# Kernel optimization log

Measured on AMD Instinct MI355X. Metric: run time of the kernel, lower is better.

Reference implementation:

```python
import jax, jax.numpy as jnp
import numpy as np

# geomloss SamplesLoss(loss='sinkhorn') defaults: p=2, blur=0.05, scaling=0.5, debias=True
BLUR = 0.05
P = 2
SCALING = 0.5
EPS_TGT = BLUR ** P            # target temperature = blur^p = 0.0025
EPS_START = 4.0                # ~ diameter^p / p for N(0,1) 3D clouds
N_FINAL = 5                    # extra iterations at target epsilon


def _eps_schedule():
    # static epsilon-annealing schedule (scaling=0.5 => eps *= 0.25 per step for p=2)
    eps, lst = EPS_START, []
    while eps > EPS_TGT:
        lst.append(eps)
        eps *= SCALING ** P
    lst += [EPS_TGT] * N_FINAL
    return jnp.asarray(lst, dtype=jnp.float32)


def _sqcost(x, y):
    # C_ij = ||x_i - y_j||^2 / 2   (geomloss p=2 cost)
    x2 = jnp.sum(x * x, axis=-1)
    y2 = jnp.sum(y * y, axis=-1)
    return 0.5 * (x2[:, None] + y2[None, :] - 2.0 * (x @ y.T))


def _ot_eps(C):
    # log-domain Sinkhorn with epsilon annealing; uniform weights
    N, M = C.shape
    la = -jnp.log(jnp.float32(N))   # log alpha_i
    lb = -jnp.log(jnp.float32(M))   # log beta_j
    f0 = jnp.zeros((N,), dtype=C.dtype)
    g0 = jnp.zeros((M,), dtype=C.dtype)

    def step(carry, eps):
        f, g = carry
        f = -eps * jax.scipy.special.logsumexp(lb + (g[None, :] - C) / eps, axis=1)
        g = -eps * jax.scipy.special.logsumexp(la + (f[:, None] - C) / eps, axis=0)
        return (f, g), None

    (f, g), _ = jax.lax.scan(jax.checkpoint(step), (f0, g0), _eps_schedule())
    # OT_eps(alpha, beta) = <alpha, f> + <beta, g> with uniform weights
    return jnp.mean(f) + jnp.mean(g)


def setup_inputs() -> dict:
    key = jax.random.key(0)
    kx, ky = jax.random.split(key)
    x = jax.random.normal(kx, (4096, 3), dtype=jnp.float32)
    y = jax.random.normal(ky, (4096, 3), dtype=jnp.float32)
    return {"x": x, "y": y}


def reference(x, y):
    # debiased Sinkhorn divergence: S = OT(x,y) - 0.5*OT(x,x) - 0.5*OT(y,y)
    oxy = _ot_eps(_sqcost(x, y))
    oxx = _ot_eps(_sqcost(x, x))
    oyy = _ot_eps(_sqcost(y, y))
    return oxy - 0.5 * oxx - 0.5 * oyy
```

## Files before the change

### kernel.cpp

```cpp
#include <hip/hip_runtime.h>
#include <math.h>

#define NPTS 4096
#define LOGN 8.317766166719343f
#define LN2f 0.6931471805599453f
#define LOG2E 1.4426950408889634f

#define NSTEPS 11
#define JSPLIT 2
#define JCHUNK (NPTS / JSPLIT)
#define RPW 8
#define RPB 32
#define NRBLK (NPTS / RPB)
#define BPP (NRBLK * JSPLIT)

typedef float f2 __attribute__((ext_vector_type(2)));
static __device__ __forceinline__ f2 mk2(float a, float b) { f2 r; r.x = a; r.y = b; return r; }

#define PC1 0.69314718f
#define PC2 0.24022651f
#define PC3 0.05550411f
#define PC4 0.00961813f
static __device__ __forceinline__ f2 pexp2(f2 d) {
    f2 n; n.x = __builtin_rintf(d.x); n.y = __builtin_rintf(d.y);
    f2 f = d - n;
    f2 p = __builtin_elementwise_fma(f, mk2(PC4, PC4), mk2(PC3, PC3));
    p = __builtin_elementwise_fma(f, p, mk2(PC2, PC2));
    p = __builtin_elementwise_fma(f, p, mk2(PC1, PC1));
    p = __builtin_elementwise_fma(f, p, mk2(1.0f, 1.0f));
    f2 r;
    r.x = __builtin_amdgcn_ldexpf(p.x, (int)n.x);
    r.y = __builtin_amdgcn_ldexpf(p.y, (int)n.y);
    return r;
}

#define PA_F2(ws)   ((float2*)(ws))
#define PB_F2(ws)   ((float2*)((ws) + 4 * NPTS))
#define PART_F2(ws) ((float2*)((ws) + 8 * NPTS))

__global__ void prep_kernel(const float* __restrict__ x, const float* __restrict__ y,
                            float* __restrict__ ws) {
    int j = blockIdx.x * 256 + threadIdx.x;
    if (j >= NPTS) return;
    float2* pa = PA_F2(ws); float2* pb = PB_F2(ws); float2* part = PART_F2(ws);
    float ax = x[3*j], ay = x[3*j+1], az = x[3*j+2];
    pa[j] = make_float2(ax, ay);
    pb[j] = make_float2(az, ax*ax + ay*ay + az*az);
    float bx = y[3*j], by = y[3*j+1], bz = y[3*j+2];
    pa[NPTS + j] = make_float2(bx, by);
    pb[NPTS + j] = make_float2(bz, bx*bx + by*by + bz*bz);
    #pragma unroll
    for (int ps = 0; ps < 6; ++ps) {
        part[(ps*2 + 0) * NPTS + j] = make_float2(12.0f, 1.0f);
        part[(ps*2 + 1) * NPTS + j] = make_float2(0.0f, 0.0f);
    }
}

__global__ void __launch_bounds__(256, 3) sinkhorn_step(float* __restrict__ ws,
        float eps, float eps_dec, int half) {
    const float2* pa = PA_F2(ws);
    const float2* pb = PB_F2(ws);
    float2* part = PART_F2(ws);

    int bid = blockIdx.x;
    int prob = bid / BPP;
    int rem  = bid % BPP;
    int js   = rem & (JSPLIT - 1);
    int rblk = rem / JSPLIT;

    int rc, cc, in_side, out_side;
    if (half == 0) { rc = (prob == 2) ? 1 : 0; cc = (prob == 1) ? 0 : 1; in_side = 1; out_side = 0; }
    else           { rc = (prob == 1) ? 0 : 1; cc = (prob == 2) ? 1 : 0; in_side = 0; out_side = 1; }

    const float k = LOG2E / eps;
    const float nhk = -0.5f * k;
    const int jbase = js * JCHUNK;

    __shared__ float bxL[JCHUNK], byL[JCHUNK], bzL[JCHUNK], uL[JCHUNK];

    {
        const float2* part_in = part + (prob*2 + in_side) * 2 * NPTS;
        for (int i = threadIdx.x; i < JCHUNK; i += 256) {
            int j = jbase + i;
            float2 P0 = part_in[j];
            float2 P1 = part_in[NPTS + j];
            float M = fmaxf(P0.x, P1.x);
            float ssum = fmaf(P0.y, __builtin_amdgcn_exp2f(P0.x - M),
                              P1.y * __builtin_amdgcn_exp2f(P1.x - M));
            float lse2 = M + __builtin_amdgcn_logf(ssum);
            float g = -eps_dec * fmaf(LN2f, lse2, -LOGN);
            float2 A = pa[cc*NPTS + j];
            float2 B = pb[cc*NPTS + j];
            bxL[i] = A.x; byL[i] = A.y; bzL[i] = B.x;
            uL[i] = fmaf(B.y, nhk, g * k);
        }
    }
    __syncthreads();

    int wave = threadIdx.x >> 6;
    int lane = threadIdx.x & 63;
    int r0 = rblk * RPB + wave * RPW;

    float2* part_out = part + ((prob*2 + out_side) * 2 + js) * NPTS;

    f2 AX[RPW], AY[RPW], AZ[RPW];
    float rak[RPW], m[RPW], s[RPW];
    #pragma unroll
    for (int r = 0; r < RPW; ++r) {
        float2 RA = pa[rc*NPTS + r0 + r];
        float2 RB = pb[rc*NPTS + r0 + r];
        float ax = RA.x * k, ay = RA.y * k, az = RB.x * k;
        AX[r] = mk2(ax, ax); AY[r] = mk2(ay, ay); AZ[r] = mk2(az, az);
        rak[r] = nhk * RB.y;
        m[r] = -INFINITY; s[r] = 0.0f;
    }

    for (int su = 0; su < JCHUNK / 512; ++su) {
        int c0 = su * 512 + 2 * lane;
        f2 BX[4], BY[4], BZ[4], U[4];
        #pragma unroll
        for (int p = 0; p < 4; ++p) {
            int j0 = c0 + p * 128;
            BX[p] = *(const f2*)&bxL[j0];
            BY[p] = *(const f2*)&byL[j0];
            BZ[p] = *(const f2*)&bzL[j0];
            U[p]  = *(const f2*)&uL[j0];
        }
        #pragma unroll
        for (int r = 0; r < RPW; ++r) {
            f2 t0 = __builtin_elementwise_fma(AX[r], BX[0],
                     __builtin_elementwise_fma(AY[r], BY[0],
                      __builtin_elementwise_fma(AZ[r], BZ[0], U[0])));
            f2 t1 = __builtin_elementwise_fma(AX[r], BX[1],
                     __builtin_elementwise_fma(AY[r], BY[1],
                      __builtin_elementwise_fma(AZ[r], BZ[1], U[1])));
            f2 t2 = __builtin_elementwise_fma(AX[r], BX[2],
                     __builtin_elementwise_fma(AY[r], BY[2],
                      __builtin_elementwise_fma(AZ[r], BZ[2], U[2])));
            f2 t3 = __builtin_elementwise_fma(AX[r], BX[3],
                     __builtin_elementwise_fma(AY[r], BY[3],
                      __builtin_elementwise_fma(AZ[r], BZ[3], U[3])));
            f2 q = __builtin_elementwise_max(
                     __builtin_elementwise_max(t0, t1),
                     __builtin_elementwise_max(t2, t3));
            float mn = fmaxf(fmaxf(q.x, q.y), m[r]);
            float er = __builtin_amdgcn_exp2f(m[r] - mn);
            f2 mn2 = mk2(mn, mn);
            f2 e0 = pexp2(t0 - mn2);
            f2 e1 = pexp2(t1 - mn2);
            f2 e2 = pexp2(t2 - mn2);
            f2 e3 = pexp2(t3 - mn2);
            f2 acc = (e0 + e1) + (e2 + e3);
            s[r] = fmaf(s[r], er, acc.x + acc.y);
            m[r] = mn;
        }
    }

    #pragma unroll
    for (int r = 0; r < RPW; ++r) {
        float M = m[r];
        for (int off = 32; off; off >>= 1) M = fmaxf(M, __shfl_xor(M, off));
        float ss = s[r] * __builtin_amdgcn_exp2f(m[r] - M);
        for (int off = 32; off; off >>= 1) ss += __shfl_xor(ss, off);
        if (lane == 0) part_out[r0 + r] = make_float2(M + rak[r], ss);
    }
}

__global__ void finalize_kernel(const float* __restrict__ ws, float* __restrict__ out,
                                float eps) {
    const float2* part = PART_F2((float*)ws);
    int tid = threadIdx.x;
    double acc = 0.0;
    for (int idx = tid; idx < 6 * NPTS; idx += 256) {
        int ps = idx >> 12;
        int row = idx & (NPTS - 1);
        float2 P0 = part[(ps*2 + 0) * NPTS + row];
        float2 P1 = part[(ps*2 + 1) * NPTS + row];
        float M = fmaxf(P0.x, P1.x);
        float ssum = fmaf(P0.y, __builtin_amdgcn_exp2f(P0.x - M),
                          P1.y * __builtin_amdgcn_exp2f(P1.x - M));
        float lse2 = M + __builtin_amdgcn_logf(ssum);
        float dual = -eps * fmaf(LN2f, lse2, -LOGN);
        acc += ((ps < 2) ? 1.0 : -0.5) * (double)dual;
    }
    for (int off = 32; off; off >>= 1) acc += __shfl_xor(acc, off);
    __shared__ double red[4];
    int wave = tid >> 6, lane = tid & 63;
    if (lane == 0) red[wave] = acc;
    __syncthreads();
    if (tid == 0) out[0] = (float)((red[0] + red[1] + red[2] + red[3]) / (double)NPTS);
}

extern "C" void kernel_launch(void* const* d_in, const int* in_sizes, int n_in,
                              void* d_out, int out_size, void* d_ws, size_t ws_size,
                              hipStream_t stream) {
    const float* x = (const float*)d_in[0];
    const float* y = (const float*)d_in[1];
    float* ws = (float*)d_ws;
    float* out = (float*)d_out;

    prep_kernel<<<dim3((NPTS + 255) / 256), dim3(256), 0, stream>>>(x, y, ws);

    float eps_list[NSTEPS];
    for (int st = 0; st < NSTEPS; ++st)
        eps_list[st] = (st < 6) ? ldexpf(4.0f, -2 * st) : 0.0025f;

    for (int st = 0; st < NSTEPS; ++st) {
        float ep = eps_list[st];
        float ed0 = (st == 0) ? ep : eps_list[st - 1];
        sinkhorn_step<<<dim3(3 * BPP), dim3(256), 0, stream>>>(ws, ep, ed0, 0);
        sinkhorn_step<<<dim3(3 * BPP), dim3(256), 0, stream>>>(ws, ep, ep, 1);
    }

    finalize_kernel<<<dim3(1), dim3(256), 0, stream>>>(ws, out, eps_list[NSTEPS - 1]);
}
```

Measured before the change: 516.7 us.

## Split columns four ways, use hardware exp2, raise occupancy

Raises the column split from two to four, so the grid doubles, each block stages half as much into shared memory, and each row carries four partial logsumexp results that are merged in the next step and in finalize. The software polynomial exp2 in the inner loop is replaced by the hardware exp2 instruction. The launch-bounds occupancy hint goes from 3 to 6 blocks. The trade is more partial-result traffic and merge work and possible register pressure at the higher occupancy target, against more parallelism and a different balance between the transcendental unit and the FMA pipe.

```diff
diff --git a/kernel.cpp b/kernel.cpp
--- a/kernel.cpp
+++ b/kernel.cpp
@@ -7,7 +7,7 @@
 #define LOG2E 1.4426950408889634f
 
 #define NSTEPS 11
-#define JSPLIT 2
+#define JSPLIT 4
 #define JCHUNK (NPTS / JSPLIT)
 #define RPW 8
 #define RPB 32
@@ -16,23 +16,6 @@
 
 typedef float f2 __attribute__((ext_vector_type(2)));
 static __device__ __forceinline__ f2 mk2(float a, float b) { f2 r; r.x = a; r.y = b; return r; }
-
-#define PC1 0.69314718f
-#define PC2 0.24022651f
-#define PC3 0.05550411f
-#define PC4 0.00961813f
-static __device__ __forceinline__ f2 pexp2(f2 d) {
-    f2 n; n.x = __builtin_rintf(d.x); n.y = __builtin_rintf(d.y);
-    f2 f = d - n;
-    f2 p = __builtin_elementwise_fma(f, mk2(PC4, PC4), mk2(PC3, PC3));
-    p = __builtin_elementwise_fma(f, p, mk2(PC2, PC2));
-    p = __builtin_elementwise_fma(f, p, mk2(PC1, PC1));
-    p = __builtin_elementwise_fma(f, p, mk2(1.0f, 1.0f));
-    f2 r;
-    r.x = __builtin_amdgcn_ldexpf(p.x, (int)n.x);
-    r.y = __builtin_amdgcn_ldexpf(p.y, (int)n.y);
-    return r;
-}
 
 #define PA_F2(ws)   ((float2*)(ws))
 #define PB_F2(ws)   ((float2*)((ws) + 4 * NPTS))
@@ -51,12 +34,14 @@
     pb[NPTS + j] = make_float2(bz, bx*bx + by*by + bz*bz);
     #pragma unroll
     for (int ps = 0; ps < 6; ++ps) {
-        part[(ps*2 + 0) * NPTS + j] = make_float2(12.0f, 1.0f);
-        part[(ps*2 + 1) * NPTS + j] = make_float2(0.0f, 0.0f);
-    }
-}
-
-__global__ void __launch_bounds__(256, 3) sinkhorn_step(float* __restrict__ ws,
+        #pragma unroll
+        for (int p = 0; p < JSPLIT; ++p)
+            part[(ps*JSPLIT + p) * NPTS + j] =
+                (p == 0) ? make_float2(12.0f, 1.0f) : make_float2(0.0f, 0.0f);
+    }
+}
+
+__global__ void __launch_bounds__(256, 6) sinkhorn_step(float* __restrict__ ws,
         float eps, float eps_dec, int half) {
     const float2* pa = PA_F2(ws);
     const float2* pb = PB_F2(ws);
@@ -79,14 +64,18 @@
     __shared__ float bxL[JCHUNK], byL[JCHUNK], bzL[JCHUNK], uL[JCHUNK];
 
     {
-        const float2* part_in = part + (prob*2 + in_side) * 2 * NPTS;
+        const float2* part_in = part + (prob*2 + in_side) * JSPLIT * NPTS;
         for (int i = threadIdx.x; i < JCHUNK; i += 256) {
             int j = jbase + i;
             float2 P0 = part_in[j];
             float2 P1 = part_in[NPTS + j];
-            float M = fmaxf(P0.x, P1.x);
-            float ssum = fmaf(P0.y, __builtin_amdgcn_exp2f(P0.x - M),
-                              P1.y * __builtin_amdgcn_exp2f(P1.x - M));
+            float2 P2 = part_in[2*NPTS + j];
+            float2 P3 = part_in[3*NPTS + j];
+            float M = fmaxf(fmaxf(P0.x, P1.x), fmaxf(P2.x, P3.x));
+            float ssum = P0.y * __builtin_amdgcn_exp2f(P0.x - M)
+                       + P1.y * __builtin_amdgcn_exp2f(P1.x - M)
+                       + P2.y * __builtin_amdgcn_exp2f(P2.x - M)
+                       + P3.y * __builtin_amdgcn_exp2f(P3.x - M);
             float lse2 = M + __builtin_amdgcn_logf(ssum);
             float g = -eps_dec * fmaf(LN2f, lse2, -LOGN);
             float2 A = pa[cc*NPTS + j];
@@ -101,7 +90,7 @@
     int lane = threadIdx.x & 63;
     int r0 = rblk * RPB + wave * RPW;
 
-    float2* part_out = part + ((prob*2 + out_side) * 2 + js) * NPTS;
+    float2* part_out = part + ((prob*2 + out_side) * JSPLIT + js) * NPTS;
 
     f2 AX[RPW], AY[RPW], AZ[RPW];
     float rak[RPW], m[RPW], s[RPW];
@@ -146,10 +135,12 @@
             float mn = fmaxf(fmaxf(q.x, q.y), m[r]);
             float er = __builtin_amdgcn_exp2f(m[r] - mn);
             f2 mn2 = mk2(mn, mn);
-            f2 e0 = pexp2(t0 - mn2);
-            f2 e1 = pexp2(t1 - mn2);
-            f2 e2 = pexp2(t2 - mn2);
-            f2 e3 = pexp2(t3 - mn2);
+            f2 d0 = t0 - mn2, d1 = t1 - mn2, d2 = t2 - mn2, d3 = t3 - mn2;
+            f2 e0, e1, e2, e3;
+            e0.x = __builtin_amdgcn_exp2f(d0.x); e0.y = __builtin_amdgcn_exp2f(d0.y);
+            e1.x = __builtin_amdgcn_exp2f(d1.x); e1.y = __builtin_amdgcn_exp2f(d1.y);
+            e2.x = __builtin_amdgcn_exp2f(d2.x); e2.y = __builtin_amdgcn_exp2f(d2.y);
+            e3.x = __builtin_amdgcn_exp2f(d3.x); e3.y = __builtin_amdgcn_exp2f(d3.y);
             f2 acc = (e0 + e1) + (e2 + e3);
             s[r] = fmaf(s[r], er, acc.x + acc.y);
             m[r] = mn;
@@ -174,11 +165,16 @@
     for (int idx = tid; idx < 6 * NPTS; idx += 256) {
         int ps = idx >> 12;
         int row = idx & (NPTS - 1);
-        float2 P0 = part[(ps*2 + 0) * NPTS + row];
-        float2 P1 = part[(ps*2 + 1) * NPTS + row];
-        float M = fmaxf(P0.x, P1.x);
-        float ssum = fmaf(P0.y, __builtin_amdgcn_exp2f(P0.x - M),
-                          P1.y * __builtin_amdgcn_exp2f(P1.x - M));
+        const float2* pb_ = part + ps * JSPLIT * NPTS + row;
+        float2 P0 = pb_[0];
+        float2 P1 = pb_[NPTS];
+        float2 P2 = pb_[2*NPTS];
+        float2 P3 = pb_[3*NPTS];
+        float M = fmaxf(fmaxf(P0.x, P1.x), fmaxf(P2.x, P3.x));
+        float ssum = P0.y * __builtin_amdgcn_exp2f(P0.x - M)
+                   + P1.y * __builtin_amdgcn_exp2f(P1.x - M)
+                   + P2.y * __builtin_amdgcn_exp2f(P2.x - M)
+                   + P3.y * __builtin_amdgcn_exp2f(P3.x - M);
         float lse2 = M + __builtin_amdgcn_logf(ssum);
         float dual = -eps * fmaf(LN2f, lse2, -LOGN);
         acc += ((ps < 2) ? 1.0 : -0.5) * (double)dual;
```

Result: slower. 1.051 ms (+103.4%).
